# Performance work log

Measured on AMD Instinct MI355X. Metric: run time of the kernel, lower is better.

## Reference

```python
import jax, jax.numpy as jnp
import numpy as np

N = 100000      # nodes
E = 1600000     # edges
H = 128         # hidden_channels
G = 128         # graphs in batch
L = 3           # num_layers
C = 4           # num_classes
BN_EPS = 1e-5


def setup_inputs() -> dict:
    key = jax.random.key(0)
    ks = jax.random.split(key, 24)
    s = 0.05
    x = jax.random.randint(ks[0], (N, 3), 0, 5, dtype=jnp.int64)
    edge_index = jax.random.randint(ks[1], (2, E), 0, N, dtype=jnp.int64)
    batch = jnp.sort(jax.random.randint(ks[2], (N,), 0, G, dtype=jnp.int64))
    p = lambda k, shp: jax.random.normal(k, shp, dtype=jnp.float32) * s
    return {
        'x': x, 'edge_index': edge_index, 'batch': batch,
        'node_emb': p(ks[3], (5, H)),
        'comp_emb': p(ks[4], (6, H)),
        'pin_emb':  p(ks[5], (6, H)),
        'proj_w': p(ks[6], (3 * H, H)), 'proj_b': p(ks[7], (H,)),
        'gin_w1': p(ks[8], (L, H, 2 * H)), 'gin_b1': p(ks[9], (L, 2 * H)),
        'gin_w2': p(ks[10], (L, 2 * H, H)), 'gin_b2': p(ks[11], (L, H)),
        'bn_gamma': jnp.ones((L, H), jnp.float32),
        'bn_beta': jnp.zeros((L, H), jnp.float32),
        'fus_w1': p(ks[12], (3 * H, 2 * H)), 'fus_b1': p(ks[13], (2 * H,)),
        'fus_w2': p(ks[14], (2 * H, H)), 'fus_b2': p(ks[15], (H,)),
        'cls_w': p(ks[16], (H, C)), 'cls_b': p(ks[17], (C,)),
    }


def _encoder(x, edge_index, batch, node_emb, comp_emb, pin_emb, proj_w, proj_b,
             gin_w1, gin_b1, gin_w2, gin_b2, bn_gamma, bn_beta):
    # embedding concat + projection
    idx = jnp.clip(x, 0, None)
    h = jnp.concatenate([node_emb[idx[:, 0]], comp_emb[idx[:, 1]], pin_emb[idx[:, 2]]], axis=1)
    h = h @ proj_w + proj_b                      # [N, H]
    src, dst = edge_index[0], edge_index[1]
    for i in range(L):
        # GINConv (eps=0): MLP(x + sum_{j->i} x_j)
        agg = jax.ops.segment_sum(h[src], dst, num_segments=N)
        z = h + agg
        z = jax.nn.relu(z @ gin_w1[i] + gin_b1[i]) @ gin_w2[i] + gin_b2[i]
        # BatchNorm1d (training-mode batch statistics), ReLU, residual
        mu = jnp.mean(z, axis=0)
        var = jnp.mean((z - mu) ** 2, axis=0)
        z = (z - mu) * jax.lax.rsqrt(var + BN_EPS) * bn_gamma[i] + bn_beta[i]
        z = jax.nn.relu(z)
        if i > 0:
            z = z + h
        h = z  # dropout = identity (eval)
    # global mean / max / sum pooling
    counts = jax.ops.segment_sum(jnp.ones((N,), h.dtype), batch, num_segments=G)
    gsum = jax.ops.segment_sum(h, batch, num_segments=G)
    gmean = gsum / jnp.maximum(counts, 1.0)[:, None]
    gmax = jax.ops.segment_max(h, batch, num_segments=G)
    gmax = jnp.where(jnp.isfinite(gmax), gmax, 0.0)
    return jnp.concatenate([gmean, gmax, gsum], axis=1)  # [G, 3H]


def reference(x, edge_index, batch, node_emb, comp_emb, pin_emb, proj_w, proj_b,
              gin_w1, gin_b1, gin_w2, gin_b2, bn_gamma, bn_beta,
              fus_w1, fus_b1, fus_w2, fus_b2, cls_w, cls_b):
    emb = _encoder(x, edge_index, batch, node_emb, comp_emb, pin_emb, proj_w, proj_b,
                   gin_w1, gin_b1, gin_w2, gin_b2, bn_gamma, bn_beta)
    f = jax.nn.relu(emb @ fus_w1 + fus_b1)
    f = jax.nn.relu(f @ fus_w2 + fus_b2)
    return f @ cls_w + cls_b                     # [G, C] logits
```

## Files before the change

kernel.cpp:

```cpp
#include <hip/hip_runtime.h>
#include <hip/hip_bf16.h>


#define NN 100000
#define NE 1600000
#define HD 128
#define NG 128
#define NL 3
#define BN_EPS 1e-5f
#define MPAD 100096
#define PCH 8

typedef unsigned short u16;
typedef unsigned int u32;
typedef __attribute__((ext_vector_type(8))) short short8v;
typedef __attribute__((ext_vector_type(4))) float f32x4;

__device__ inline u16 bf16_hi(float v) {
    __hip_bfloat16 h = __float2bfloat16(v);
    return *(u16*)&h;
}
__device__ inline float bf16_f(u16 u) {
    __hip_bfloat16 h = *(__hip_bfloat16*)&u;
    return __bfloat162float(h);
}
__device__ inline void split_bf16(float v, u16* hi, u16* lo) {
    u16 h = bf16_hi(v);
    *hi = h;
    *lo = bf16_hi(v - bf16_f(h));
}

__device__ inline void gload_lds16(const void* g, void* l) {
    __builtin_amdgcn_global_load_lds(
        (const __attribute__((address_space(1))) void*)g,
        (__attribute__((address_space(3))) void*)l, 16, 0, 0);
}

__global__ void proj_tables_kernel(const float* __restrict__ node_emb,
                                   const float* __restrict__ comp_emb,
                                   const float* __restrict__ pin_emb,
                                   const float* __restrict__ proj_w,
                                   float* __restrict__ P) {
    int c = threadIdx.x;
    for (int r = 0; r < 17; ++r) {
        const float* emb;
        int base;
        if (r < 5)        { emb = node_emb + r * HD;        base = 0; }
        else if (r < 11)  { emb = comp_emb + (r - 5) * HD;  base = HD; }
        else              { emb = pin_emb + (r - 11) * HD;  base = 2 * HD; }
        float acc = 0.f;
        for (int k = 0; k < HD; ++k)
            acc += emb[k] * proj_w[(size_t)(base + k) * HD + c];
        P[r * HD + c] = acc;
    }
}

__global__ __launch_bounds__(256) void embed_kernel(const int* __restrict__ x,
                                                    const float* __restrict__ P,
                                                    const float* __restrict__ proj_b,
                                                    float* __restrict__ h,
                                                    u16* __restrict__ hb) {
    int i = blockIdx.x * 256 + threadIdx.x;
    int n = i >> 5;
    if (n >= NN) return;
    int c4 = (i & 31) * 4;
    int i0 = x[3 * n + 0]; i0 = i0 < 0 ? 0 : (i0 > 4 ? 4 : i0);
    int i1 = x[3 * n + 1]; i1 = i1 < 0 ? 0 : (i1 > 5 ? 5 : i1);
    int i2 = x[3 * n + 2]; i2 = i2 < 0 ? 0 : (i2 > 5 ? 5 : i2);
    float4 a = *(const float4*)(P + i0 * HD + c4);
    float4 b = *(const float4*)(P + (5 + i1) * HD + c4);
    float4 c = *(const float4*)(P + (11 + i2) * HD + c4);
    float4 bb = *(const float4*)(proj_b + c4);
    float4 o;
    o.x = a.x + b.x + c.x + bb.x;
    o.y = a.y + b.y + c.y + bb.y;
    o.z = a.z + b.z + c.z + bb.z;
    o.w = a.w + b.w + c.w + bb.w;
    *(float4*)(h + (size_t)n * HD + c4) = o;
    ushort4 s;
    s.x = bf16_hi(o.x); s.y = bf16_hi(o.y); s.z = bf16_hi(o.z); s.w = bf16_hi(o.w);
    *(ushort4*)(hb + (size_t)n * HD + c4) = s;
}

__global__ void hist_kernel(const int* __restrict__ dst, int* __restrict__ deg,
                            int* __restrict__ rank) {
    int e = blockIdx.x * 256 + threadIdx.x;
    if (e < NE) rank[e] = atomicAdd(&deg[dst[e]], 1);
}

__global__ __launch_bounds__(256) void scan1_kernel(const int* __restrict__ deg,
                                                    int* __restrict__ rowstart,
                                                    int* __restrict__ partials) {
    __shared__ int arr[256];
    int blk = blockIdx.x, t = threadIdx.x;
    int base = blk * 2048 + t * 8;
    int v[8];
    int s = 0;
#pragma unroll
    for (int j = 0; j < 8; ++j) {
        int idx = base + j;
        int d = (idx < NN) ? deg[idx] : 0;
        v[j] = s;
        s += d;
    }
    int own = s;
    arr[t] = s;
    __syncthreads();
    for (int off = 1; off < 256; off <<= 1) {
        int add = (t >= off) ? arr[t - off] : 0;
        __syncthreads();
        arr[t] += add;
        __syncthreads();
    }
    int excl = arr[t] - own;
#pragma unroll
    for (int j = 0; j < 8; ++j) {
        int idx = base + j;
        if (idx < NN) rowstart[idx] = excl + v[j];
    }
    if (t == 255) partials[blk] = arr[255];
}

__global__ void scan2_kernel(int* __restrict__ partials, int* __restrict__ rowstart, int nblk) {
    if (threadIdx.x == 0) {
        int run = 0;
        for (int b = 0; b < nblk; ++b) {
            int p = partials[b];
            partials[b] = run;
            run += p;
        }
        rowstart[NN] = run;
    }
}

__global__ void scan3_kernel(int* __restrict__ rowstart, const int* __restrict__ partials) {
    int i = blockIdx.x * 256 + threadIdx.x;
    if (i < NN) rowstart[i] += partials[i >> 11];
}

__global__ void fill_kernel(const int* __restrict__ src, const int* __restrict__ dst,
                            const int* __restrict__ rowstart, const int* __restrict__ rank,
                            int* __restrict__ csr_src) {
    int e = blockIdx.x * 256 + threadIdx.x;
    if (e < NE) csr_src[rowstart[dst[e]] + rank[e]] = src[e];
}

__global__ __launch_bounds__(256) void segsum_kernel(const float* __restrict__ h,
                                                     const u16* __restrict__ hb,
                                                     const int* __restrict__ rowstart,
                                                     const int* __restrict__ csr_src,
                                                     u16* __restrict__ zhi,
                                                     u16* __restrict__ zlo) {
    int wid = (blockIdx.x * 256 + threadIdx.x) >> 6;
    int lane = threadIdx.x & 63;
    if (wid >= NN) return;
    int beg = __builtin_amdgcn_readfirstlane(rowstart[wid]);
    int end = __builtin_amdgcn_readfirstlane(rowstart[wid + 1]);
    const float2* hp = (const float2*)h;
    float2 acc = hp[(size_t)wid * 64 + lane];
    const ushort2* hbp = (const ushort2*)hb;
    for (int base = beg; base < end; base += 64) {
        int cnt = end - base;
        if (cnt > 64) cnt = 64;
        int idx = (lane < cnt) ? csr_src[base + lane] : 0;
        int j = 0;
        for (; j + 8 <= cnt; j += 8) {
            int s0 = __shfl(idx, j);
            int s1 = __shfl(idx, j + 1);
            int s2 = __shfl(idx, j + 2);
            int s3 = __shfl(idx, j + 3);
            int s4 = __shfl(idx, j + 4);
            int s5 = __shfl(idx, j + 5);
            int s6 = __shfl(idx, j + 6);
            int s7 = __shfl(idx, j + 7);
            ushort2 v0 = hbp[(size_t)s0 * 64 + lane];
            ushort2 v1 = hbp[(size_t)s1 * 64 + lane];
            ushort2 v2 = hbp[(size_t)s2 * 64 + lane];
            ushort2 v3 = hbp[(size_t)s3 * 64 + lane];
            ushort2 v4 = hbp[(size_t)s4 * 64 + lane];
            ushort2 v5 = hbp[(size_t)s5 * 64 + lane];
            ushort2 v6 = hbp[(size_t)s6 * 64 + lane];
            ushort2 v7 = hbp[(size_t)s7 * 64 + lane];
            acc.x += bf16_f(v0.x); acc.y += bf16_f(v0.y);
            acc.x += bf16_f(v1.x); acc.y += bf16_f(v1.y);
            acc.x += bf16_f(v2.x); acc.y += bf16_f(v2.y);
            acc.x += bf16_f(v3.x); acc.y += bf16_f(v3.y);
            acc.x += bf16_f(v4.x); acc.y += bf16_f(v4.y);
            acc.x += bf16_f(v5.x); acc.y += bf16_f(v5.y);
            acc.x += bf16_f(v6.x); acc.y += bf16_f(v6.y);
            acc.x += bf16_f(v7.x); acc.y += bf16_f(v7.y);
        }
        for (; j < cnt; ++j) {
            int s = __shfl(idx, j);
            ushort2 v = hbp[(size_t)s * 64 + lane];
            acc.x += bf16_f(v.x);
            acc.y += bf16_f(v.y);
        }
    }
    u16 h0, l0, h1, l1;
    split_bf16(acc.x, &h0, &l0);
    split_bf16(acc.y, &h1, &l1);
    ushort2 vh; vh.x = h0; vh.y = h1;
    ushort2 vl; vl.x = l0; vl.y = l1;
    ((ushort2*)zhi)[(size_t)wid * 64 + lane] = vh;
    ((ushort2*)zlo)[(size_t)wid * 64 + lane] = vl;
}

__global__ __launch_bounds__(256) void prep_weights_kernel(const float* __restrict__ gw1,
                                                           const float* __restrict__ gw2,
                                                           u16* __restrict__ w1hi, u16* __restrict__ w1lo,
                                                           u16* __restrict__ w2hi, u16* __restrict__ w2lo) {
    int i = blockIdx.x * 256 + threadIdx.x;
    if (i >= NL * 32768) return;
    int l = i / 32768, rem = i % 32768;
    int n1 = rem >> 7, k1 = rem & 127;
    split_bf16(gw1[(size_t)l * 32768 + (size_t)k1 * 256 + n1], &w1hi[i], &w1lo[i]);
    int n2 = rem >> 8, k2 = rem & 255;
    split_bf16(gw2[(size_t)l * 32768 + (size_t)k2 * 128 + n2], &w2hi[i], &w2lo[i]);
}

__global__ __launch_bounds__(256) void gin_mlp(const u16* __restrict__ zH, const u16* __restrict__ zL,
                                               const u16* __restrict__ W1h, const u16* __restrict__ W1l,
                                               const u16* __restrict__ W2h, const u16* __restrict__ W2l,
                                               const float* __restrict__ b1, const float* __restrict__ b2,
                                               float* __restrict__ Of, float* __restrict__ sums) {
    __shared__ __align__(16) u16 zh[8192], zl[8192];
    __shared__ __align__(16) u16 z1h[8192], z1l[8192];
    const int t = threadIdx.x;
    const int wv = t >> 6, lane = t & 63;
    const int l15 = lane & 15, l4 = lane >> 4;
    const int m0 = blockIdx.x * 64;

    {
        int rlo = lane >> 4;
        int cpos = lane & 15;
        for (int i = 0; i < 4; ++i) {
            int lrow = wv * 16 + i * 4 + rlo;
            int sc = cpos ^ (lrow & 15);
            gload_lds16(zH + (size_t)(m0 + lrow) * 128 + sc * 8, zh + wv * 2048 + i * 512);
            gload_lds16(zL + (size_t)(m0 + lrow) * 128 + sc * 8, zl + wv * 2048 + i * 512);
        }
    }
    __syncthreads();

    f32x4 a2[4][2];
#pragma unroll
    for (int m = 0; m < 4; ++m)
#pragma unroll
        for (int n = 0; n < 2; ++n)
            a2[m][n] = (f32x4){0.f, 0.f, 0.f, 0.f};

    for (int half = 0; half < 2; ++half) {
        f32x4 a1[4][2];
#pragma unroll
        for (int m = 0; m < 4; ++m)
#pragma unroll
            for (int n = 0; n < 2; ++n)
                a1[m][n] = (f32x4){0.f, 0.f, 0.f, 0.f};

#pragma unroll
        for (int ks = 0; ks < 4; ++ks) {
            short8v ah[4], al[4];
#pragma unroll
            for (int m = 0; m < 4; ++m) {
                int rA = m * 16 + l15;
                int au = rA * 128 + (((ks * 4 + l4) ^ (rA & 15)) << 3);
                ah[m] = *(const short8v*)(zh + au);
                al[m] = *(const short8v*)(zl + au);
            }
#pragma unroll
            for (int n = 0; n < 2; ++n) {
                int col = half * 128 + wv * 32 + n * 16 + l15;
                short8v bh = *(const short8v*)(W1h + (size_t)col * 128 + ks * 32 + l4 * 8);
                short8v bl = *(const short8v*)(W1l + (size_t)col * 128 + ks * 32 + l4 * 8);
#pragma unroll
                for (int m = 0; m < 4; ++m) {
                    a1[m][n] = __builtin_amdgcn_mfma_f32_16x16x32_bf16(ah[m], bh, a1[m][n], 0, 0, 0);
                    a1[m][n] = __builtin_amdgcn_mfma_f32_16x16x32_bf16(ah[m], bl, a1[m][n], 0, 0, 0);
                    a1[m][n] = __builtin_amdgcn_mfma_f32_16x16x32_bf16(al[m], bh, a1[m][n], 0, 0, 0);
                }
            }
        }
        __syncthreads();
#pragma unroll
        for (int n = 0; n < 2; ++n) {
            int colL = wv * 32 + n * 16 + l15;
            float bv = b1[half * 128 + colL];
#pragma unroll
            for (int m = 0; m < 4; ++m) {
#pragma unroll
                for (int r = 0; r < 4; ++r) {
                    int row = m * 16 + l4 * 4 + r;
                    float v = fmaxf(a1[m][n][r] + bv, 0.f);
                    u16 hi, lo;
                    split_bf16(v, &hi, &lo);
                    int addr = row * 128 + (((colL >> 3) ^ (row & 15)) << 3) + (colL & 7);
                    z1h[addr] = hi;
                    z1l[addr] = lo;
                }
            }
        }
        __syncthreads();
#pragma unroll
        for (int ks = 0; ks < 4; ++ks) {
            short8v ah[4], al[4];
#pragma unroll
            for (int m = 0; m < 4; ++m) {
                int rA = m * 16 + l15;
                int au = rA * 128 + (((ks * 4 + l4) ^ (rA & 15)) << 3);
                ah[m] = *(const short8v*)(z1h + au);
                al[m] = *(const short8v*)(z1l + au);
            }
#pragma unroll
            for (int n = 0; n < 2; ++n) {
                int col = wv * 32 + n * 16 + l15;
                int kk = half * 128 + ks * 32 + l4 * 8;
                short8v bh = *(const short8v*)(W2h + (size_t)col * 256 + kk);
                short8v bl = *(const short8v*)(W2l + (size_t)col * 256 + kk);
#pragma unroll
                for (int m = 0; m < 4; ++m) {
                    a2[m][n] = __builtin_amdgcn_mfma_f32_16x16x32_bf16(ah[m], bh, a2[m][n], 0, 0, 0);
                    a2[m][n] = __builtin_amdgcn_mfma_f32_16x16x32_bf16(ah[m], bl, a2[m][n], 0, 0, 0);
                    a2[m][n] = __builtin_amdgcn_mfma_f32_16x16x32_bf16(al[m], bh, a2[m][n], 0, 0, 0);
                }
            }
        }
    }

#pragma unroll
    for (int n = 0; n < 2; ++n) {
        int gcol = wv * 32 + n * 16 + l15;
        float bv = b2[gcol];
        float s = 0.f, q = 0.f;
#pragma unroll
        for (int m = 0; m < 4; ++m) {
#pragma unroll
            for (int r = 0; r < 4; ++r) {
                int grow = m0 + m * 16 + l4 * 4 + r;
                float v = a2[m][n][r] + bv;
                Of[(size_t)grow * HD + gcol] = v;
                if (grow < NN) { s += v; q += v * v; }
            }
        }
        s += __shfl_xor(s, 16); s += __shfl_xor(s, 32);
        q += __shfl_xor(q, 16); q += __shfl_xor(q, 32);
        if (l4 == 0) {
            atomicAdd(&sums[gcol], s);
            atomicAdd(&sums[128 + gcol], q);
        }
    }
}

__global__ void bn_finalize_kernel(const float* __restrict__ sums,
                                   const float* __restrict__ gamma,
                                   const float* __restrict__ beta,
                                   float* __restrict__ scale, float* __restrict__ shift) {
    int c = threadIdx.x;
    float mean = sums[c] / (float)NN;
    float var = sums[128 + c] / (float)NN - mean * mean;
    float rstd = rsqrtf(fmaxf(var, 0.f) + BN_EPS);
    float sc = rstd * gamma[c];
    scale[c] = sc;
    shift[c] = beta[c] - mean * sc;
}

__global__ __launch_bounds__(256) void bn_apply_kernel(const float* __restrict__ z2,
                                                       const float* __restrict__ scale,
                                                       const float* __restrict__ shift,
                                                       float* __restrict__ h,
                                                       u16* __restrict__ hb, int use_res) {
    int i = blockIdx.x * 256 + threadIdx.x;
    if (i >= NN * 32) return;
    int c4 = (i & 31) * 4;
    float4 v = ((const float4*)z2)[i];
    float4 sc = *(const float4*)(scale + c4);
    float4 sh = *(const float4*)(shift + c4);
    float4 o;
    o.x = fmaxf(v.x * sc.x + sh.x, 0.f);
    o.y = fmaxf(v.y * sc.y + sh.y, 0.f);
    o.z = fmaxf(v.z * sc.z + sh.z, 0.f);
    o.w = fmaxf(v.w * sc.w + sh.w, 0.f);
    if (use_res) {
        float4 r = ((float4*)h)[i];
        o.x += r.x; o.y += r.y; o.z += r.z; o.w += r.w;
    }
    ((float4*)h)[i] = o;
    ushort4 s;
    s.x = bf16_hi(o.x); s.y = bf16_hi(o.y); s.z = bf16_hi(o.z); s.w = bf16_hi(o.w);
    ((ushort4*)hb)[i] = s;
}

__global__ __launch_bounds__(256) void pool_part_kernel(const float* __restrict__ h,
                                                        const int* __restrict__ batch,
                                                        float* __restrict__ psum,
                                                        float* __restrict__ pmax) {
    __shared__ int bounds[2];
    __shared__ float redS[256], redM[256];
    int g = blockIdx.x, chunk = blockIdx.y, t = threadIdx.x;
    if (t < 2) {
        int target = g + t, lo = 0, hi = NN;
        while (lo < hi) {
            int mid = (lo + hi) >> 1;
            if (batch[mid] < target) lo = mid + 1;
            else hi = mid;
        }
        bounds[t] = lo;
    }
    __syncthreads();
    int lo = bounds[0], hi = bounds[1], len = hi - lo;
    int c0 = lo + (len * chunk) / PCH;
    int c1 = lo + (len * (chunk + 1)) / PCH;
    int c = t & 127, half = t >> 7;
    float s = 0.f, m = -3.4e38f;
    for (int r = c0 + half; r < c1; r += 2) {
        float v = h[(size_t)r * HD + c];
        s += v;
        m = fmaxf(m, v);
    }
    redS[t] = s;
    redM[t] = m;
    __syncthreads();
    if (t < 128) {
        psum[((size_t)g * PCH + chunk) * HD + t] = redS[t] + redS[t + 128];
        pmax[((size_t)g * PCH + chunk) * HD + t] = fmaxf(redM[t], redM[t + 128]);
    }
}

__global__ __launch_bounds__(128) void pool_combine_kernel(const float* __restrict__ psum,
                                                           const float* __restrict__ pmax,
                                                           const int* __restrict__ batch,
                                                           float* __restrict__ emb) {
    __shared__ int bounds[2];
    int g = blockIdx.x, t = threadIdx.x;
    if (t < 2) {
        int target = g + t, lo = 0, hi = NN;
        while (lo < hi) {
            int mid = (lo + hi) >> 1;
            if (batch[mid] < target) lo = mid + 1;
            else hi = mid;
        }
        bounds[t] = lo;
    }
    __syncthreads();
    int len = bounds[1] - bounds[0];
    float s = 0.f, m = -3.4e38f;
#pragma unroll
    for (int ch = 0; ch < PCH; ++ch) {
        s += psum[((size_t)g * PCH + ch) * HD + t];
        m = fmaxf(m, pmax[((size_t)g * PCH + ch) * HD + t]);
    }
    float mean;
    if (len > 0) {
        mean = s / (float)len;
    } else {
        mean = 0.f; m = 0.f; s = 0.f;
    }
    emb[g * 384 + t] = mean;
    emb[g * 384 + 128 + t] = m;
    emb[g * 384 + 256 + t] = s;
}

__global__ __launch_bounds__(256) void head_kernel(const float* __restrict__ emb,
                                                   const float* __restrict__ w1, const float* __restrict__ b1,
                                                   const float* __restrict__ w2, const float* __restrict__ b2,
                                                   const float* __restrict__ cw, const float* __restrict__ cb,
                                                   float* __restrict__ out) {
    __shared__ float e[384], f1[256], f2[128];
    int g = blockIdx.x, t = threadIdx.x;
    e[t] = emb[g * 384 + t];
    if (t < 128) e[256 + t] = emb[g * 384 + 256 + t];
    __syncthreads();
    float acc = b1[t];
    for (int k = 0; k < 384; ++k) acc += e[k] * w1[(size_t)k * 256 + t];
    f1[t] = fmaxf(acc, 0.f);
    __syncthreads();
    if (t < 128) {
        float a2 = b2[t];
        for (int k = 0; k < 256; ++k) a2 += f1[k] * w2[k * 128 + t];
        f2[t] = fmaxf(a2, 0.f);
    }
    __syncthreads();
    if (t < 4) {
        float a3 = cb[t];
        for (int k = 0; k < 128; ++k) a3 += f2[k] * cw[k * 4 + t];
        out[g * 4 + t] = a3;
    }
}

extern "C" void kernel_launch(void* const* d_in, const int* in_sizes, int n_in,
                              void* d_out, int out_size, void* d_ws, size_t ws_size,
                              hipStream_t stream) {
    const int* x = (const int*)d_in[0];
    const int* edge = (const int*)d_in[1];
    const int* batch = (const int*)d_in[2];
    const float* node_emb = (const float*)d_in[3];
    const float* comp_emb = (const float*)d_in[4];
    const float* pin_emb = (const float*)d_in[5];
    const float* proj_w = (const float*)d_in[6];
    const float* proj_b = (const float*)d_in[7];
    const float* gin_w1 = (const float*)d_in[8];
    const float* gin_b1 = (const float*)d_in[9];
    const float* gin_w2 = (const float*)d_in[10];
    const float* gin_b2 = (const float*)d_in[11];
    const float* bn_gamma = (const float*)d_in[12];
    const float* bn_beta = (const float*)d_in[13];
    const float* fus_w1 = (const float*)d_in[14];
    const float* fus_b1 = (const float*)d_in[15];
    const float* fus_w2 = (const float*)d_in[16];
    const float* fus_b2 = (const float*)d_in[17];
    const float* cls_w = (const float*)d_in[18];
    const float* cls_b = (const float*)d_in[19];

    const int* esrc = edge;
    const int* edst = edge + NE;

    char* ws = (char*)d_ws;
    size_t off = 0;
    auto alloc = [&](size_t bytes) -> void* {
        void* p = ws + off;
        off = (off + bytes + 255) & ~(size_t)255;
        return p;
    };
    float* h = (float*)alloc((size_t)NN * HD * 4);
    u16* hb = (u16*)alloc((size_t)NN * HD * 2);
    u16* z_hi = (u16*)alloc((size_t)MPAD * HD * 2);
    u16* z_lo = (u16*)alloc((size_t)MPAD * HD * 2);
    float* z2 = (float*)alloc((size_t)MPAD * HD * 4);
    u16* w1hi = (u16*)alloc((size_t)NL * 32768 * 2);
    u16* w1lo = (u16*)alloc((size_t)NL * 32768 * 2);
    u16* w2hi = (u16*)alloc((size_t)NL * 32768 * 2);
    u16* w2lo = (u16*)alloc((size_t)NL * 32768 * 2);
    float* P = (float*)alloc(17 * HD * 4);
    float* sums = (float*)alloc(256 * 4);
    float* scale = (float*)alloc(HD * 4);
    float* shift = (float*)alloc(HD * 4);
    float* emb = (float*)alloc((size_t)NG * 384 * 4);
    float* psum = (float*)alloc((size_t)NG * PCH * HD * 4);
    float* pmax = (float*)alloc((size_t)NG * PCH * HD * 4);
    int* deg = (int*)alloc((size_t)NN * 4);
    int* rowstart = (int*)alloc((size_t)(NN + 1) * 4);
    int* rank = (int*)alloc((size_t)NE * 4);
    int* csr_src = (int*)alloc((size_t)NE * 4);
    int* partials = (int*)alloc(64 * 4);

    proj_tables_kernel<<<1, 128, 0, stream>>>(node_emb, comp_emb, pin_emb, proj_w, P);
    embed_kernel<<<(NN * 32 + 255) / 256, 256, 0, stream>>>(x, P, proj_b, h, hb);
    prep_weights_kernel<<<(NL * 32768 + 255) / 256, 256, 0, stream>>>(gin_w1, gin_w2,
                                                                      w1hi, w1lo, w2hi, w2lo);

    hipMemsetAsync(deg, 0, (size_t)NN * 4, stream);
    hist_kernel<<<(NE + 255) / 256, 256, 0, stream>>>(edst, deg, rank);
    int nblk = (NN + 2047) / 2048;
    scan1_kernel<<<nblk, 256, 0, stream>>>(deg, rowstart, partials);
    scan2_kernel<<<1, 64, 0, stream>>>(partials, rowstart, nblk);
    scan3_kernel<<<(NN + 255) / 256, 256, 0, stream>>>(rowstart, partials);
    fill_kernel<<<(NE + 255) / 256, 256, 0, stream>>>(esrc, edst, rowstart, rank, csr_src);

    const int gm = MPAD / 64;
    for (int l = 0; l < NL; ++l) {
        segsum_kernel<<<(NN * 64 + 255) / 256, 256, 0, stream>>>(h, hb, rowstart, csr_src, z_hi, z_lo);
        hipMemsetAsync(sums, 0, 256 * 4, stream);
        gin_mlp<<<gm, 256, 0, stream>>>(z_hi, z_lo,
                                        w1hi + (size_t)l * 32768, w1lo + (size_t)l * 32768,
                                        w2hi + (size_t)l * 32768, w2lo + (size_t)l * 32768,
                                        gin_b1 + (size_t)l * 256, gin_b2 + (size_t)l * HD,
                                        z2, sums);
        bn_finalize_kernel<<<1, 128, 0, stream>>>(sums, bn_gamma + l * HD, bn_beta + l * HD, scale, shift);
        bn_apply_kernel<<<(NN * 32 + 255) / 256, 256, 0, stream>>>(z2, scale, shift, h, hb, l > 0 ? 1 : 0);
    }

    pool_part_kernel<<<dim3(NG, PCH), 256, 0, stream>>>(h, batch, psum, pmax);
    pool_combine_kernel<<<NG, 128, 0, stream>>>(psum, pmax, batch, emb);
    head_kernel<<<NG, 256, 0, stream>>>(emb, fus_w1, fus_b1, fus_w2, fus_b2, cls_w, cls_b,
                                        (float*)d_out);
}
```

Before: 896.3 us.

## Store hidden activations as single bf16 and prefetch GIN weights into registers

The intermediate ReLU output of the first GIN linear layer is now written to LDS as a single bf16 value instead of a hi/lo split pair. This halves LDS traffic for that buffer and drops one of three MFMAs per tile in the second GEMM. All W1 and W2 fragments are loaded into registers early, overlapping the global loads with the LDS fill, and the two-half loop is manually unrolled. The trade-offs are lower accuracy on the hidden activation and much higher register pressure, which may reduce occupancy or cause spills.

```diff
diff --git a/kernel.cpp b/kernel.cpp
--- a/kernel.cpp
+++ b/kernel.cpp
@@ -225,7 +225,7 @@
                                                const float* __restrict__ b1, const float* __restrict__ b2,
                                                float* __restrict__ Of, float* __restrict__ sums) {
     __shared__ __align__(16) u16 zh[8192], zl[8192];
-    __shared__ __align__(16) u16 z1h[8192], z1l[8192];
+    __shared__ __align__(16) u16 z1b[8192];
     const int t = threadIdx.x;
     const int wv = t >> 6, lane = t & 63;
     const int l15 = lane & 15, l4 = lane >> 4;
@@ -241,6 +241,18 @@
             gload_lds16(zL + (size_t)(m0 + lrow) * 128 + sc * 8, zl + wv * 2048 + i * 512);
         }
     }
+
+    short8v w1h_[2][4][2], w1l_[2][4][2];
+#pragma unroll
+    for (int hf = 0; hf < 2; ++hf)
+#pragma unroll
+        for (int ks = 0; ks < 4; ++ks)
+#pragma unroll
+            for (int n = 0; n < 2; ++n) {
+                int col = hf * 128 + wv * 32 + n * 16 + l15;
+                w1h_[hf][ks][n] = *(const short8v*)(W1h + (size_t)col * 128 + ks * 32 + l4 * 8);
+                w1l_[hf][ks][n] = *(const short8v*)(W1l + (size_t)col * 128 + ks * 32 + l4 * 8);
+            }
     __syncthreads();
 
     f32x4 a2[4][2];
@@ -250,81 +262,141 @@
         for (int n = 0; n < 2; ++n)
             a2[m][n] = (f32x4){0.f, 0.f, 0.f, 0.f};
 
-    for (int half = 0; half < 2; ++half) {
-        f32x4 a1[4][2];
+    short8v w2h0[4][2], w2l0[4][2];
+#pragma unroll
+    for (int ks = 0; ks < 4; ++ks)
+#pragma unroll
+        for (int n = 0; n < 2; ++n) {
+            int col = wv * 32 + n * 16 + l15;
+            w2h0[ks][n] = *(const short8v*)(W2h + (size_t)col * 256 + ks * 32 + l4 * 8);
+            w2l0[ks][n] = *(const short8v*)(W2l + (size_t)col * 256 + ks * 32 + l4 * 8);
+        }
+
+    f32x4 a1[4][2];
+#pragma unroll
+    for (int m = 0; m < 4; ++m)
+#pragma unroll
+        for (int n = 0; n < 2; ++n)
+            a1[m][n] = (f32x4){0.f, 0.f, 0.f, 0.f};
+#pragma unroll
+    for (int ks = 0; ks < 4; ++ks) {
+        short8v ah[4], al[4];
+#pragma unroll
+        for (int m = 0; m < 4; ++m) {
+            int rA = m * 16 + l15;
+            int au = rA * 128 + (((ks * 4 + l4) ^ (rA & 15)) << 3);
+            ah[m] = *(const short8v*)(zh + au);
+            al[m] = *(const short8v*)(zl + au);
+        }
+#pragma unroll
+        for (int n = 0; n < 2; ++n)
+#pragma unroll
+            for (int m = 0; m < 4; ++m) {
+                a1[m][n] = __builtin_amdgcn_mfma_f32_16x16x32_bf16(ah[m], w1h_[0][ks][n], a1[m][n], 0, 0, 0);
+                a1[m][n] = __builtin_amdgcn_mfma_f32_16x16x32_bf16(ah[m], w1l_[0][ks][n], a1[m][n], 0, 0, 0);
+                a1[m][n] = __builtin_amdgcn_mfma_f32_16x16x32_bf16(al[m], w1h_[0][ks][n], a1[m][n], 0, 0, 0);
+            }
+    }
+    __syncthreads();
+#pragma unroll
+    for (int n = 0; n < 2; ++n) {
+        int colL = wv * 32 + n * 16 + l15;
+        float bv = b1[colL];
 #pragma unroll
         for (int m = 0; m < 4; ++m)
 #pragma unroll
-            for (int n = 0; n < 2; ++n)
-                a1[m][n] = (f32x4){0.f, 0.f, 0.f, 0.f};
-
-#pragma unroll
-        for (int ks = 0; ks < 4; ++ks) {
-            short8v ah[4], al[4];
+            for (int r = 0; r < 4; ++r) {
+                int row = m * 16 + l4 * 4 + r;
+                float v = fmaxf(a1[m][n][r] + bv, 0.f);
+                int addr = row * 128 + (((colL >> 3) ^ (row & 15)) << 3) + (colL & 7);
+                z1b[addr] = bf16_hi(v);
+            }
+    }
+    __syncthreads();
+
+    short8v w2h1[4][2], w2l1[4][2];
+#pragma unroll
+    for (int ks = 0; ks < 4; ++ks)
+#pragma unroll
+        for (int n = 0; n < 2; ++n) {
+            int col = wv * 32 + n * 16 + l15;
+            w2h1[ks][n] = *(const short8v*)(W2h + (size_t)col * 256 + 128 + ks * 32 + l4 * 8);
+            w2l1[ks][n] = *(const short8v*)(W2l + (size_t)col * 256 + 128 + ks * 32 + l4 * 8);
+        }
+
+#pragma unroll
+    for (int ks = 0; ks < 4; ++ks) {
+        short8v p[4];
+#pragma unroll
+        for (int m = 0; m < 4; ++m) {
+            int rA = m * 16 + l15;
+            int au = rA * 128 + (((ks * 4 + l4) ^ (rA & 15)) << 3);
+            p[m] = *(const short8v*)(z1b + au);
+        }
+#pragma unroll
+        for (int n = 0; n < 2; ++n)
 #pragma unroll
             for (int m = 0; m < 4; ++m) {
-                int rA = m * 16 + l15;
-                int au = rA * 128 + (((ks * 4 + l4) ^ (rA & 15)) << 3);
-                ah[m] = *(const short8v*)(zh + au);
-                al[m] = *(const short8v*)(zl + au);
-            }
-#pragma unroll
-            for (int n = 0; n < 2; ++n) {
-                int col = half * 128 + wv * 32 + n * 16 + l15;
-                short8v bh = *(const short8v*)(W1h + (size_t)col * 128 + ks * 32 + l4 * 8);
-                short8v bl = *(const short8v*)(W1l + (size_t)col * 128 + ks * 32 + l4 * 8);
-#pragma unroll
-                for (int m = 0; m < 4; ++m) {
-                    a1[m][n] = __builtin_amdgcn_mfma_f32_16x16x32_bf16(ah[m], bh, a1[m][n], 0, 0, 0);
-                    a1[m][n] = __builtin_amdgcn_mfma_f32_16x16x32_bf16(ah[m], bl, a1[m][n], 0, 0, 0);
-                    a1[m][n] = __builtin_amdgcn_mfma_f32_16x16x32_bf16(al[m], bh, a1[m][n], 0, 0, 0);
-                }
-            }
-        }
-        __syncthreads();
-#pragma unroll
-        for (int n = 0; n < 2; ++n) {
-            int colL = wv * 32 + n * 16 + l15;
-            float bv = b1[half * 128 + colL];
+                a2[m][n] = __builtin_amdgcn_mfma_f32_16x16x32_bf16(p[m], w2h0[ks][n], a2[m][n], 0, 0, 0);
+                a2[m][n] = __builtin_amdgcn_mfma_f32_16x16x32_bf16(p[m], w2l0[ks][n], a2[m][n], 0, 0, 0);
+            }
+    }
+#pragma unroll
+    for (int m = 0; m < 4; ++m)
+#pragma unroll
+        for (int n = 0; n < 2; ++n)
+            a1[m][n] = (f32x4){0.f, 0.f, 0.f, 0.f};
+#pragma unroll
+    for (int ks = 0; ks < 4; ++ks) {
+        short8v ah[4], al[4];
+#pragma unroll
+        for (int m = 0; m < 4; ++m) {
+            int rA = m * 16 + l15;
+            int au = rA * 128 + (((ks * 4 + l4) ^ (rA & 15)) << 3);
+            ah[m] = *(const short8v*)(zh + au);
+            al[m] = *(const short8v*)(zl + au);
+        }
+#pragma unroll
+        for (int n = 0; n < 2; ++n)
 #pragma unroll
             for (int m = 0; m < 4; ++m) {
-#pragma unroll
-                for (int r = 0; r < 4; ++r) {
-                    int row = m * 16 + l4 * 4 + r;
-                    float v = fmaxf(a1[m][n][r] + bv, 0.f);
-                    u16 hi, lo;
-                    split_bf16(v, &hi, &lo);
-                    int addr = row * 128 + (((colL >> 3) ^ (row & 15)) << 3) + (colL & 7);
-                    z1h[addr] = hi;
-                    z1l[addr] = lo;
-                }
-            }
-        }
-        __syncthreads();
-#pragma unroll
-        for (int ks = 0; ks < 4; ++ks) {
-            short8v ah[4], al[4];
+                a1[m][n] = __builtin_amdgcn_mfma_f32_16x16x32_bf16(ah[m], w1h_[1][ks][n], a1[m][n], 0, 0, 0);
+                a1[m][n] = __builtin_amdgcn_mfma_f32_16x16x32_bf16(ah[m], w1l_[1][ks][n], a1[m][n], 0, 0, 0);
+                a1[m][n] = __builtin_amdgcn_mfma_f32_16x16x32_bf16(al[m], w1h_[1][ks][n], a1[m][n], 0, 0, 0);
+            }
+    }
+    __syncthreads();
+#pragma unroll
+    for (int n = 0; n < 2; ++n) {
+        int colL = wv * 32 + n * 16 + l15;
+        float bv = b1[128 + colL];
+#pragma unroll
+        for (int m = 0; m < 4; ++m)
+#pragma unroll
+            for (int r = 0; r < 4; ++r) {
+                int row = m * 16 + l4 * 4 + r;
+                float v = fmaxf(a1[m][n][r] + bv, 0.f);
+                int addr = row * 128 + (((colL >> 3) ^ (row & 15)) << 3) + (colL & 7);
+                z1b[addr] = bf16_hi(v);
+            }
+    }
+    __syncthreads();
+#pragma unroll
+    for (int ks = 0; ks < 4; ++ks) {
+        short8v p[4];
+#pragma unroll
+        for (int m = 0; m < 4; ++m) {
+            int rA = m * 16 + l15;
+            int au = rA * 128 + (((ks * 4 + l4) ^ (rA & 15)) << 3);
+            p[m] = *(const short8v*)(z1b + au);
+        }
+#pragma unroll
+        for (int n = 0; n < 2; ++n)
 #pragma unroll
             for (int m = 0; m < 4; ++m) {
-                int rA = m * 16 + l15;
-                int au = rA * 128 + (((ks * 4 + l4) ^ (rA & 15)) << 3);
-                ah[m] = *(const short8v*)(z1h + au);
-                al[m] = *(const short8v*)(z1l + au);
-            }
-#pragma unroll
-            for (int n = 0; n < 2; ++n) {
-                int col = wv * 32 + n * 16 + l15;
-                int kk = half * 128 + ks * 32 + l4 * 8;
-                short8v bh = *(const short8v*)(W2h + (size_t)col * 256 + kk);
-                short8v bl = *(const short8v*)(W2l + (size_t)col * 256 + kk);
-#pragma unroll
-                for (int m = 0; m < 4; ++m) {
-                    a2[m][n] = __builtin_amdgcn_mfma_f32_16x16x32_bf16(ah[m], bh, a2[m][n], 0, 0, 0);
-                    a2[m][n] = __builtin_amdgcn_mfma_f32_16x16x32_bf16(ah[m], bl, a2[m][n], 0, 0, 0);
-                    a2[m][n] = __builtin_amdgcn_mfma_f32_16x16x32_bf16(al[m], bh, a2[m][n], 0, 0, 0);
-                }
-            }
-        }
+                a2[m][n] = __builtin_amdgcn_mfma_f32_16x16x32_bf16(p[m], w2h1[ks][n], a2[m][n], 0, 0, 0);
+                a2[m][n] = __builtin_amdgcn_mfma_f32_16x16x32_bf16(p[m], w2l1[ks][n], a2[m][n], 0, 0, 0);
+            }
     }
 
 #pragma unroll
```

Result: no change. 905.2 us (+1.0%).
